# Kernel tuning notes

Hardware: AMD Instinct MI355X
Metric: run time of the kernel (lower is better)

## Reference

```python
import jax, jax.numpy as jnp
import numpy as np

NEG_BIG = 1e20


def setup_inputs() -> dict:
    key = jax.random.key(0)
    k1, k2, k3 = jax.random.split(key, 3)
    B, Tenc, Tdec, D = 8, 2048, 512, 1024
    enc = jax.random.normal(k1, (B, Tenc, D), dtype=jnp.float32)
    dec = jax.random.normal(k2, (B, Tdec, D), dtype=jnp.float32)
    enc_mask = jax.random.randint(k3, (B, Tenc), 0, 2, dtype=jnp.int32)
    # guarantee at least one valid position per row to keep softmax well-defined
    enc_mask = enc_mask.at[:, 0].set(1)
    return {"enc": enc, "enc_mask": enc_mask, "dec": dec}


def reference(enc, enc_mask, dec):
    # dropout=0 and identity transforms -> enc_trans = enc, dec_trans = dec
    mask = enc_mask.astype(enc.dtype)  # (B, Tenc)
    # raw scores: sum_d dec[b,u,d] * enc[b,t,d] -> (B, Tenc, Tdec)
    raw = jnp.einsum('btd,bud->btu', enc, dec)
    raw = raw - (1.0 - mask)[:, :, None] * NEG_BIG
    scores = jax.nn.softmax(raw, axis=1)  # softmax over Tenc
    # context: sum_t scores[b,t,u] * enc[b,t,d] -> (B, Tdec, D)
    context = jnp.einsum('btu,btd->bud', scores, enc)
    return context, scores
```

## Files before the change

### kernel.cpp

```cpp
#include <hip/hip_runtime.h>
#include <math.h>

#define BATCH 8
#define TENC 2048
#define TDEC 512
#define DIM 1024
#define NEG_BIG 1e20f

typedef __attribute__((ext_vector_type(8))) short short8;
typedef __attribute__((ext_vector_type(4))) float f32x4;
typedef unsigned short ushort_t;

__device__ __forceinline__ unsigned int bf16rn(float x) {
    unsigned int u = __float_as_uint(x);
    return (u + 0x7FFFu + ((u >> 16) & 1u)) >> 16;
}
__device__ __forceinline__ float bf16f(unsigned int b) {
    return __uint_as_float(b << 16);
}
__device__ __forceinline__ void split2(float x, unsigned int& h, unsigned int& l) {
    h = bf16rn(x);
    l = bf16rn(x - bf16f(h));
}

#define GLOAD16(g, l)                                                        \
    __builtin_amdgcn_global_load_lds(                                        \
        (const __attribute__((address_space(1))) unsigned int*)(g),          \
        (__attribute__((address_space(3))) unsigned int*)(l), 16, 0, 0)

__device__ __forceinline__ size_t tiled_off(int row, int k, int ntK) {
    return ((size_t)(row >> 4) * ntK + (k >> 5)) * 512
         + ((k >> 3) & 3) * 128 + (row & 15) * 8;
}


__global__ __launch_bounds__(256) void prep_fused(
    const float* __restrict__ enc, const float* __restrict__ dec,
    ushort_t* __restrict__ encH, ushort_t* __restrict__ encL,
    ushort_t* __restrict__ encT, ushort_t* __restrict__ decH,
    ushort_t* __restrict__ decL)
{
    __shared__ ushort_t T[64][72];

    const int b   = blockIdx.z;
    const int d0  = blockIdx.x * 64;
    const int tid = threadIdx.x;

    if (blockIdx.y < 32) {
        const int t0 = blockIdx.y * 64;
        const float* E = enc + (size_t)b * TENC * DIM;
        const size_t bofs1 = (size_t)b * TENC * DIM;
        const size_t bofs2 = (size_t)b * DIM * TENC;

        const int ltr = tid >> 2;
#pragma unroll
        for (int it = 0; it < 2; ++it) {
            const int c  = (tid & 3) + it * 4;
            const int gt = t0 + ltr;
            const int gd = d0 + c * 8;
            float4 x0 = *(const float4*)&E[(size_t)gt * DIM + gd];
            float4 x1 = *(const float4*)&E[(size_t)gt * DIM + gd + 4];
            float xs[8] = {x0.x, x0.y, x0.z, x0.w, x1.x, x1.y, x1.z, x1.w};
            unsigned int h[8], l[8];
            short8 hv, lv;
#pragma unroll
            for (int j = 0; j < 8; ++j) {
                split2(xs[j], h[j], l[j]);
                hv[j] = (short)h[j];
                lv[j] = (short)l[j];
            }
            const size_t off = bofs1 + tiled_off(gt, gd, DIM / 32);
            *(short8*)&encH[off] = hv;
            *(short8*)&encL[off] = lv;
#pragma unroll
            for (int j = 0; j < 8; ++j) T[c * 8 + j][ltr] = (ushort_t)h[j];
        }
        __syncthreads();

        const int dr = tid >> 2;
#pragma unroll
        for (int it = 0; it < 2; ++it) {
            const int tc = (tid & 3) + it * 4;
            const int gd = d0 + dr;
            const int gt = t0 + tc * 8;
            short8 v = *(const short8*)&T[dr][tc * 8];
            *(short8*)&encT[bofs2 + tiled_off(gd, gt, TENC / 32)] = v;
        }
    } else {
        const int u0 = (blockIdx.y - 32) * 64;
        const float* D = dec + (size_t)b * TDEC * DIM;
        const size_t bofs = (size_t)b * TDEC * DIM;

        const int lur = tid >> 2;
#pragma unroll
        for (int it = 0; it < 2; ++it) {
            const int c  = (tid & 3) + it * 4;
            const int gu = u0 + lur;
            const int gd = d0 + c * 8;
            float4 x0 = *(const float4*)&D[(size_t)gu * DIM + gd];
            float4 x1 = *(const float4*)&D[(size_t)gu * DIM + gd + 4];
            float xs[8] = {x0.x, x0.y, x0.z, x0.w, x1.x, x1.y, x1.z, x1.w};
            short8 hv, lv;
#pragma unroll
            for (int j = 0; j < 8; ++j) {
                unsigned int h, l;
                split2(xs[j], h, l);
                hv[j] = (short)h;
                lv[j] = (short)l;
            }
            const size_t off = bofs + tiled_off(gu, gd, DIM / 32);
            *(short8*)&decH[off] = hv;
            *(short8*)&decL[off] = lv;
        }
    }
}

__global__ __launch_bounds__(256) void gemm1_lds(
    const ushort_t* __restrict__ encH, const ushort_t* __restrict__ encL,
    const ushort_t* __restrict__ decH, const ushort_t* __restrict__ decL,
    const int* __restrict__ mask, float* __restrict__ raw,
    float* __restrict__ pm, float* __restrict__ ps)
{
    __shared__ __align__(16) ushort_t Ah[128 * 32];
    __shared__ __align__(16) ushort_t Al[128 * 32];
    __shared__ __align__(16) ushort_t Bh[128 * 32];
    __shared__ __align__(16) ushort_t Bl[128 * 32];
    __shared__ float smx[4][68];
    __shared__ float ssx[4][68];

    const int b  = blockIdx.z;
    const int m0 = blockIdx.y * 128;
    const int n0 = blockIdx.x * 128;
    const int tid = threadIdx.x;

    const int lane = tid & 63;
    const int w    = tid >> 6;
    const int wm   = (w & 1) * 64;
    const int wn   = (w >> 1) * 64;
    const int lr   = lane & 15;
    const int q    = lane >> 4;
    const int l8   = lane * 8;

    const int fa = wm * 32 + q * 128 + lr * 8;
    const int fb = wn * 32 + q * 128 + lr * 8;

    const ushort_t* AH = encH + (size_t)b * TENC * DIM;
    const ushort_t* AL = encL + (size_t)b * TENC * DIM;
    const ushort_t* BH = decH + (size_t)b * TDEC * DIM;
    const ushort_t* BL = decL + (size_t)b * TDEC * DIM;
    float* C = raw + (size_t)b * TENC * TDEC;

    f32x4 acc[4][4] = {};

    for (int k0 = 0; k0 < DIM; k0 += 32) {
        __syncthreads();
#pragma unroll
        for (int q2 = 0; q2 < 2; ++q2) {
            const int rg = w * 2 + q2;
            const size_t tA = ((size_t)((m0 >> 4) + rg) * (DIM / 32) + (k0 >> 5)) * 512 + l8;
            const size_t tB = ((size_t)((n0 >> 4) + rg) * (DIM / 32) + (k0 >> 5)) * 512 + l8;
            GLOAD16(AH + tA, &Ah[rg * 512]);
            GLOAD16(AL + tA, &Al[rg * 512]);
            GLOAD16(BH + tB, &Bh[rg * 512]);
            GLOAD16(BL + tB, &Bl[rg * 512]);
        }
        __syncthreads();

        short8 ah[4], al[4], bh[4], bl[4];
#pragma unroll
        for (int i = 0; i < 4; ++i) {
            ah[i] = *(const short8*)&Ah[fa + i * 512];
            al[i] = *(const short8*)&Al[fa + i * 512];
            bh[i] = *(const short8*)&Bh[fb + i * 512];
            bl[i] = *(const short8*)&Bl[fb + i * 512];
        }
#pragma unroll
        for (int i = 0; i < 4; ++i)
#pragma unroll
            for (int j = 0; j < 4; ++j) {
                acc[i][j] = __builtin_amdgcn_mfma_f32_16x16x32_bf16(ah[i], bh[j], acc[i][j], 0, 0, 0);
                acc[i][j] = __builtin_amdgcn_mfma_f32_16x16x32_bf16(ah[i], bl[j], acc[i][j], 0, 0, 0);
                acc[i][j] = __builtin_amdgcn_mfma_f32_16x16x32_bf16(al[i], bh[j], acc[i][j], 0, 0, 0);
            }
    }

    float mkv[4][4];
#pragma unroll
    for (int i = 0; i < 4; ++i)
#pragma unroll
        for (int rr = 0; rr < 4; ++rr) {
            const int t = m0 + wm + i * 16 + q * 4 + rr;
            mkv[i][rr] = (mask[b * TENC + t] == 0) ? NEG_BIG : 0.0f;
        }

    float cm[4] = {-INFINITY, -INFINITY, -INFINITY, -INFINITY};
    float cs[4] = {0.f, 0.f, 0.f, 0.f};
#pragma unroll
    for (int i = 0; i < 4; ++i)
#pragma unroll
        for (int rr = 0; rr < 4; ++rr) {
            const int t = m0 + wm + i * 16 + q * 4 + rr;
#pragma unroll
            for (int j = 0; j < 4; ++j) {
                const int u = n0 + wn + j * 16 + lr;
                const float v = acc[i][j][rr] - mkv[i][rr];
                C[(size_t)t * TDEC + u] = v;
                cm[j] = fmaxf(cm[j], v);
            }
        }
#pragma unroll
    for (int i = 0; i < 4; ++i)
#pragma unroll
        for (int rr = 0; rr < 4; ++rr)
#pragma unroll
            for (int j = 0; j < 4; ++j)
                cs[j] += __expf(acc[i][j][rr] - mkv[i][rr] - cm[j]);

#pragma unroll
    for (int j = 0; j < 4; ++j) {
#pragma unroll
        for (int d = 16; d < 64; d <<= 1) {
            float om = __shfl_xor(cm[j], d, 64);
            float os = __shfl_xor(cs[j], d, 64);
            float mn = fmaxf(cm[j], om);
            cs[j] = cs[j] * __expf(cm[j] - mn) + os * __expf(om - mn);
            cm[j] = mn;
        }
    }

    if (q == 0) {
#pragma unroll
        for (int j = 0; j < 4; ++j) {
            smx[w][j * 16 + lr] = cm[j];
            ssx[w][j * 16 + lr] = cs[j];
        }
    }
    __syncthreads();
    if (tid < 128) {
        const int col = tid;
        const int wp  = (col >> 6) * 2;
        const int ci  = col & 63;
        const float m1 = smx[wp][ci],     s1 = ssx[wp][ci];
        const float m2 = smx[wp + 1][ci], s2 = ssx[wp + 1][ci];
        const float M = fmaxf(m1, m2);
        const float S = s1 * __expf(m1 - M) + s2 * __expf(m2 - M);
        const int idx = b * TDEC + n0 + col;
        const int tb  = m0 >> 7;
        pm[(size_t)tb * (BATCH * TDEC) + idx] = M;
        ps[(size_t)tb * (BATCH * TDEC) + idx] = S;
    }
}

__global__ __launch_bounds__(256) void norm_kernel(
    float* __restrict__ S, const float* __restrict__ pm,
    const float* __restrict__ ps, ushort_t* __restrict__ scoresT)
{
    __shared__ ushort_t T[64][72];
    __shared__ float cMs[64], cIs[64];

    const int b  = blockIdx.z;
    const int t0 = blockIdx.x * 64;
    const int u0 = blockIdx.y * 64;
    const int tid = threadIdx.x;

    if (tid < 64) {
        const int idx = b * TDEC + u0 + tid;
        float M = -INFINITY;
#pragma unroll
        for (int z = 0; z < 16; ++z)
            M = fmaxf(M, pm[(size_t)z * (BATCH * TDEC) + idx]);
        float s = 0.0f;
#pragma unroll
        for (int z = 0; z < 16; ++z)
            s += ps[(size_t)z * (BATCH * TDEC) + idx] *
                 __expf(pm[(size_t)z * (BATCH * TDEC) + idx] - M);
        cMs[tid] = M;
        cIs[tid] = 1.0f / s;
    }
    __syncthreads();

    const int tr  = tid >> 4;
    const int ucl = (tid & 15) * 4;

    float4 M4 = *(const float4*)&cMs[ucl];
    float4 I4 = *(const float4*)&cIs[ucl];

    float* base = S + (size_t)b * TENC * TDEC;

#pragma unroll
    for (int i = 0; i < 4; ++i) {
        const int t = t0 + tr + 16 * i;
        float4 x = *(const float4*)&base[(size_t)t * TDEC + u0 + ucl];
        float4 p;
        p.x = __expf(x.x - M4.x) * I4.x;
        p.y = __expf(x.y - M4.y) * I4.y;
        p.z = __expf(x.z - M4.z) * I4.z;
        p.w = __expf(x.w - M4.w) * I4.w;
        *(float4*)&base[(size_t)t * TDEC + u0 + ucl] = p;
        const int tloc = tr + 16 * i;
        T[ucl + 0][tloc] = (ushort_t)bf16rn(p.x);
        T[ucl + 1][tloc] = (ushort_t)bf16rn(p.y);
        T[ucl + 2][tloc] = (ushort_t)bf16rn(p.z);
        T[ucl + 3][tloc] = (ushort_t)bf16rn(p.w);
    }
    __syncthreads();

    const size_t bofs = (size_t)b * TDEC * TENC;
    const int ur = tid >> 2;
#pragma unroll
    for (int it = 0; it < 2; ++it) {
        const int tc = (tid & 3) + it * 4;
        const int gu = u0 + ur;
        const int gt = t0 + tc * 8;
        short8 v = *(const short8*)&T[ur][tc * 8];
        *(short8*)&scoresT[bofs + tiled_off(gu, gt, TENC / 32)] = v;
    }
}

__global__ __launch_bounds__(256) void gemm2_lds(
    const ushort_t* __restrict__ scoresT, const ushort_t* __restrict__ encT,
    float* __restrict__ p0, float* __restrict__ p1,
    float* __restrict__ p2, float* __restrict__ p3)
{
    __shared__ __align__(16) ushort_t Ah[128 * 32];
    __shared__ __align__(16) ushort_t Bh[128 * 32];

    const int b  = blockIdx.z >> 2;
    const int ks = blockIdx.z & 3;
    const int m0 = blockIdx.y * 128;
    const int n0 = blockIdx.x * 128;
    const int tid = threadIdx.x;

    const int lane = tid & 63;
    const int w    = tid >> 6;
    const int wm   = (w & 1) * 64;
    const int wn   = (w >> 1) * 64;
    const int lr   = lane & 15;
    const int q    = lane >> 4;
    const int l8   = lane * 8;

    const int fa = wm * 32 + q * 128 + lr * 8;
    const int fb = wn * 32 + q * 128 + lr * 8;

    const ushort_t* A = scoresT + (size_t)b * TDEC * TENC;
    const ushort_t* B = encT    + (size_t)b * DIM * TENC;
    float* Psel = ks == 0 ? p0 : (ks == 1 ? p1 : (ks == 2 ? p2 : p3));
    float* P = Psel + (size_t)b * TDEC * DIM;

    const int kbeg = ks * (TENC / 4);
    const int kend = kbeg + TENC / 4;

    f32x4 acc[4][4] = {};

    for (int k0 = kbeg; k0 < kend; k0 += 32) {
        __syncthreads();
#pragma unroll
        for (int q2 = 0; q2 < 2; ++q2) {
            const int rg = w * 2 + q2;
            const size_t tA = ((size_t)((m0 >> 4) + rg) * (TENC / 32) + (k0 >> 5)) * 512 + l8;
            const size_t tB = ((size_t)((n0 >> 4) + rg) * (TENC / 32) + (k0 >> 5)) * 512 + l8;
            GLOAD16(A + tA, &Ah[rg * 512]);
            GLOAD16(B + tB, &Bh[rg * 512]);
        }
        __syncthreads();

        short8 ah[4], bh[4];
#pragma unroll
        for (int i = 0; i < 4; ++i) {
            ah[i] = *(const short8*)&Ah[fa + i * 512];
            bh[i] = *(const short8*)&Bh[fb + i * 512];
        }
#pragma unroll
        for (int i = 0; i < 4; ++i)
#pragma unroll
            for (int j = 0; j < 4; ++j)
                acc[i][j] = __builtin_amdgcn_mfma_f32_16x16x32_bf16(ah[i], bh[j], acc[i][j], 0, 0, 0);
    }

#pragma unroll
    for (int i = 0; i < 4; ++i)
#pragma unroll
        for (int rr = 0; rr < 4; ++rr) {
            const int u = m0 + wm + i * 16 + q * 4 + rr;
#pragma unroll
            for (int j = 0; j < 4; ++j) {
                const int d = n0 + wn + j * 16 + lr;
                P[(size_t)u * DIM + d] = acc[i][j][rr];
            }
        }
}

__global__ __launch_bounds__(256) void reduce_ctx(
    const float* __restrict__ p0, const float* __restrict__ p1,
    const float* __restrict__ p2, const float* __restrict__ p3,
    float* __restrict__ ctx)
{
    const size_t i4 = ((size_t)blockIdx.x * 256 + threadIdx.x) * 4;
    float4 a = *(const float4*)(p0 + i4);
    float4 b = *(const float4*)(p1 + i4);
    float4 c = *(const float4*)(p2 + i4);
    float4 d = *(const float4*)(p3 + i4);
    float4 o;
    o.x = a.x + b.x + c.x + d.x;
    o.y = a.y + b.y + c.y + d.y;
    o.z = a.z + b.z + c.z + d.z;
    o.w = a.w + b.w + c.w + d.w;
    *(float4*)(ctx + i4) = o;
}


__device__ __forceinline__ void store8(ushort_t* ph, ushort_t* pl,
                                       float4 x0, float4 x1) {
    float xs[8] = {x0.x, x0.y, x0.z, x0.w, x1.x, x1.y, x1.z, x1.w};
    short8 hv, lv;
#pragma unroll
    for (int i = 0; i < 8; ++i) {
        unsigned int h, l;
        split2(xs[i], h, l);
        hv[i] = (short)h;
        lv[i] = (short)l;
    }
    *(short8*)ph = hv;
    *(short8*)pl = lv;
}

__device__ __forceinline__ void wr4(ushort_t* ph, ushort_t* pl, const float* x) {
    unsigned int h[4], l[4];
#pragma unroll
    for (int i = 0; i < 4; ++i) split2(x[i], h[i], l[i]);
    *(uint2*)ph = make_uint2(h[0] | (h[1] << 16), h[2] | (h[3] << 16));
    *(uint2*)pl = make_uint2(l[0] | (l[1] << 16), l[2] | (l[3] << 16));
}

__device__ __forceinline__ short8 frag8B(const ushort_t* p) {
    union { short8 v; uint2 u[2]; } f;
    f.u[0] = *(const uint2*)p;
    f.u[1] = *(const uint2*)(p + 4);
    return f.v;
}

__global__ __launch_bounds__(256) void gemm1_mfma(
    const float* __restrict__ enc, const float* __restrict__ dec,
    const int* __restrict__ mask, float* __restrict__ raw)
{
    __shared__ __align__(16) ushort_t Ah[128 * 32];
    __shared__ __align__(16) ushort_t Al[128 * 32];
    __shared__ __align__(16) ushort_t Bh[128 * 32];
    __shared__ __align__(16) ushort_t Bl[128 * 32];

    const int b  = blockIdx.z;
    const int m0 = blockIdx.y * 128;
    const int n0 = blockIdx.x * 128;
    const int tid = threadIdx.x;

    const float* A  = enc + (size_t)b * TENC * DIM;
    const float* Bg = dec + (size_t)b * TDEC * DIM;
    float*       C  = raw + (size_t)b * TENC * TDEC;

    const int lane = tid & 63;
    const int wv   = tid >> 6;
    const int wm   = (wv & 1) * 64;
    const int wn   = (wv >> 1) * 64;
    const int lr   = lane & 15;
    const int q    = lane >> 4;

    const int r0 = tid >> 2;
    const int c8 = (tid & 3) * 8;

    f32x4 acc[4][4] = {};

    for (int k0 = 0; k0 < DIM; k0 += 32) {
        const float* pa0 = A  + (size_t)(m0 + r0) * DIM + k0 + c8;
        const float* pa1 = A  + (size_t)(m0 + r0 + 64) * DIM + k0 + c8;
        const float* pb0 = Bg + (size_t)(n0 + r0) * DIM + k0 + c8;
        const float* pb1 = Bg + (size_t)(n0 + r0 + 64) * DIM + k0 + c8;
        float4 a0 = *(const float4*)pa0, a0b = *(const float4*)(pa0 + 4);
        float4 a1 = *(const float4*)pa1, a1b = *(const float4*)(pa1 + 4);
        float4 b0 = *(const float4*)pb0, b0b = *(const float4*)(pb0 + 4);
        float4 b1 = *(const float4*)pb1, b1b = *(const float4*)(pb1 + 4);

        __syncthreads();
        store8(&Ah[r0 * 32 + c8],        &Al[r0 * 32 + c8],        a0, a0b);
        store8(&Ah[(r0 + 64) * 32 + c8], &Al[(r0 + 64) * 32 + c8], a1, a1b);
        store8(&Bh[r0 * 32 + c8],        &Bl[r0 * 32 + c8],        b0, b0b);
        store8(&Bh[(r0 + 64) * 32 + c8], &Bl[(r0 + 64) * 32 + c8], b1, b1b);
        __syncthreads();

        short8 ah[4], al[4], bh[4], bl[4];
#pragma unroll
        for (int i = 0; i < 4; ++i) {
            ah[i] = *(const short8*)&Ah[(wm + i * 16 + lr) * 32 + q * 8];
            al[i] = *(const short8*)&Al[(wm + i * 16 + lr) * 32 + q * 8];
            bh[i] = *(const short8*)&Bh[(wn + i * 16 + lr) * 32 + q * 8];
            bl[i] = *(const short8*)&Bl[(wn + i * 16 + lr) * 32 + q * 8];
        }
#pragma unroll
        for (int i = 0; i < 4; ++i)
#pragma unroll
            for (int j = 0; j < 4; ++j) {
                acc[i][j] = __builtin_amdgcn_mfma_f32_16x16x32_bf16(ah[i], bh[j], acc[i][j], 0, 0, 0);
                acc[i][j] = __builtin_amdgcn_mfma_f32_16x16x32_bf16(ah[i], bl[j], acc[i][j], 0, 0, 0);
                acc[i][j] = __builtin_amdgcn_mfma_f32_16x16x32_bf16(al[i], bh[j], acc[i][j], 0, 0, 0);
            }
    }

#pragma unroll
    for (int i = 0; i < 4; ++i)
#pragma unroll
        for (int rr = 0; rr < 4; ++rr) {
            const int t = m0 + wm + i * 16 + q * 4 + rr;
            const float mk = (mask[b * TENC + t] == 0) ? NEG_BIG : 0.0f;
#pragma unroll
            for (int j = 0; j < 4; ++j) {
                const int u = n0 + wn + j * 16 + lr;
                C[(size_t)t * TDEC + u] = acc[i][j][rr] - mk;
            }
        }
}

__global__ __launch_bounds__(256) void softmax_kernel(float* __restrict__ S)
{
    const int b  = blockIdx.y;
    const int u0 = blockIdx.x * 16;
    const int up = threadIdx.x & 15;
    const int tg = threadIdx.x >> 4;

    float* col = S + (size_t)b * TENC * TDEC + u0;

    float m = -INFINITY, s = 0.0f;
    for (int t = tg; t < TENC; t += 16) {
        float x = col[(size_t)t * TDEC + up];
        float mn = fmaxf(m, x);
        s = s * __expf(m - mn) + __expf(x - mn);
        m = mn;
    }

    __shared__ float sm[16][17];
    __shared__ float ss[16][17];
    sm[tg][up] = m;
    ss[tg][up] = s;
    __syncthreads();

    float M = -INFINITY;
#pragma unroll
    for (int j = 0; j < 16; ++j) M = fmaxf(M, sm[j][up]);
    float sum = 0.0f;
#pragma unroll
    for (int j = 0; j < 16; ++j) sum += ss[j][up] * __expf(sm[j][up] - M);
    const float inv = 1.0f / sum;

    for (int t = tg; t < TENC; t += 16) {
        float x = col[(size_t)t * TDEC + up];
        col[(size_t)t * TDEC + up] = __expf(x - M) * inv;
    }
}

#define G2_LD 36

__global__ __launch_bounds__(256) void gemm2_mfma(
    const float* __restrict__ scores, const float* __restrict__ enc,
    float* __restrict__ context)
{
    __shared__ __align__(16) ushort_t Ah[128 * G2_LD];
    __shared__ __align__(16) ushort_t Al[128 * G2_LD];
    __shared__ __align__(16) ushort_t Bh[128 * G2_LD];
    __shared__ __align__(16) ushort_t Bl[128 * G2_LD];

    const int b  = blockIdx.z;
    const int m0 = blockIdx.y * 128;
    const int n0 = blockIdx.x * 128;
    const int tid = threadIdx.x;

    const float* S = scores + (size_t)b * TENC * TDEC;
    const float* E = enc    + (size_t)b * TENC * DIM;
    float*       C = context + (size_t)b * TDEC * DIM;

    const int lane = tid & 63;
    const int wv   = tid >> 6;
    const int wm   = (wv & 1) * 64;
    const int wn   = (wv >> 1) * 64;
    const int lr   = lane & 15;
    const int q    = lane >> 4;

    const int ul = tid & 127;
    const int th = (tid >> 7) * 16;

    f32x4 acc[4][4] = {};

    for (int k0 = 0; k0 < TENC; k0 += 32) {
        float av[16], bv[16];
#pragma unroll
        for (int i = 0; i < 4; ++i) {
            const int t = k0 + th + i * 4;
#pragma unroll
            for (int j = 0; j < 4; ++j) {
                av[i * 4 + j] = S[(size_t)(t + j) * TDEC + m0 + ul];
                bv[i * 4 + j] = E[(size_t)(t + j) * DIM + n0 + ul];
            }
        }
        __syncthreads();
#pragma unroll
        for (int i = 0; i < 4; ++i) {
            const int tt = th + i * 4;
            wr4(&Ah[ul * G2_LD + tt], &Al[ul * G2_LD + tt], &av[i * 4]);
            wr4(&Bh[ul * G2_LD + tt], &Bl[ul * G2_LD + tt], &bv[i * 4]);
        }
        __syncthreads();

        short8 ah[4], al[4], bh[4], bl[4];
#pragma unroll
        for (int i = 0; i < 4; ++i) {
            ah[i] = frag8B(&Ah[(wm + i * 16 + lr) * G2_LD + q * 8]);
            al[i] = frag8B(&Al[(wm + i * 16 + lr) * G2_LD + q * 8]);
            bh[i] = frag8B(&Bh[(wn + i * 16 + lr) * G2_LD + q * 8]);
            bl[i] = frag8B(&Bl[(wn + i * 16 + lr) * G2_LD + q * 8]);
        }
#pragma unroll
        for (int i = 0; i < 4; ++i)
#pragma unroll
            for (int j = 0; j < 4; ++j) {
                acc[i][j] = __builtin_amdgcn_mfma_f32_16x16x32_bf16(ah[i], bh[j], acc[i][j], 0, 0, 0);
                acc[i][j] = __builtin_amdgcn_mfma_f32_16x16x32_bf16(ah[i], bl[j], acc[i][j], 0, 0, 0);
                acc[i][j] = __builtin_amdgcn_mfma_f32_16x16x32_bf16(al[i], bh[j], acc[i][j], 0, 0, 0);
            }
    }

#pragma unroll
    for (int i = 0; i < 4; ++i)
#pragma unroll
        for (int rr = 0; rr < 4; ++rr) {
            const int u = m0 + wm + i * 16 + q * 4 + rr;
#pragma unroll
            for (int j = 0; j < 4; ++j) {
                const int d = n0 + wn + j * 16 + lr;
                C[(size_t)u * DIM + d] = acc[i][j][rr];
            }
        }
}

extern "C" void kernel_launch(void* const* d_in, const int* in_sizes, int n_in,
                              void* d_out, int out_size, void* d_ws, size_t ws_size,
                              hipStream_t stream)
{
    const float* enc      = (const float*)d_in[0];
    const int*   enc_mask = (const int*)  d_in[1];
    const float* dec      = (const float*)d_in[2];

    float* context = (float*)d_out;
    float* scores  = context + (size_t)BATCH * TDEC * DIM;

    const size_t OFF_ENC_H = 0;
    const size_t OFF_ENC_L = 33554432;
    const size_t OFF_DEC_H = 67108864;
    const size_t OFF_DEC_L = 75497472;
    const size_t OFF_ENC_T = 83886080;
    const size_t OFF_SCO_T = 117440512;
    const size_t WS_NEED   = 134217728;

    if (ws_size >= WS_NEED) {
        char* w = (char*)d_ws;
        ushort_t* encH    = (ushort_t*)(w + OFF_ENC_H);
        ushort_t* encL    = (ushort_t*)(w + OFF_ENC_L);
        ushort_t* decH    = (ushort_t*)(w + OFF_DEC_H);
        ushort_t* decL    = (ushort_t*)(w + OFF_DEC_L);
        ushort_t* encT    = (ushort_t*)(w + OFF_ENC_T);
        ushort_t* scoresT = (ushort_t*)(w + OFF_SCO_T);
        float*    part0   = (float*)(w + OFF_ENC_H);
        float*    part1   = (float*)(w + OFF_ENC_H + 16777216);
        float*    part2   = (float*)(w + OFF_ENC_L);
        float*    part3   = (float*)(w + OFF_ENC_L + 16777216);
        float*    pm      = context;
        float*    ps      = context + 65536;

        prep_fused<<<dim3(DIM / 64, 40, BATCH), 256, 0, stream>>>(
            enc, dec, encH, encL, encT, decH, decL);

        gemm1_lds<<<dim3(TDEC / 128, TENC / 128, BATCH), 256, 0, stream>>>(
            encH, encL, decH, decL, enc_mask, scores, pm, ps);

        norm_kernel<<<dim3(TENC / 64, TDEC / 64, BATCH), 256, 0, stream>>>(
            scores, pm, ps, scoresT);

        gemm2_lds<<<dim3(DIM / 128, TDEC / 128, BATCH * 4), 256, 0, stream>>>(
            scoresT, encT, part0, part1, part2, part3);

        reduce_ctx<<<4096, 256, 0, stream>>>(part0, part1, part2, part3, context);
    } else {
        gemm1_mfma<<<dim3(TDEC / 128, TENC / 128, BATCH), 256, 0, stream>>>(
            enc, dec, enc_mask, scores);
        softmax_kernel<<<dim3(TDEC / 16, BATCH), 256, 0, stream>>>(scores);
        gemm2_mfma<<<dim3(DIM / 128, TDEC / 128, BATCH), 256, 0, stream>>>(
            scores, enc, context);
    }
}
```

Measured before the change: 243.3 us.

## Store split-K partials as bf16 and put batch on blockIdx.x

The gemm2 split-K partial sums are now written as bf16, and the reduce kernel reads and sums them as bf16. This halves the traffic for the partial buffers. The launch grids for gemm1 and gemm2 are also reordered so batch is the fastest-varying block index, which is meant to spread batches across XCDs and improve cache locality. The cost is lower precision in the context output, since each partial is rounded to bf16 before the final fp32 sum.

```diff
diff --git a/kernel.cpp b/kernel.cpp
--- a/kernel.cpp
+++ b/kernel.cpp
@@ -128,9 +128,9 @@
     __shared__ float smx[4][68];
     __shared__ float ssx[4][68];
 
-    const int b  = blockIdx.z;
+    const int b  = blockIdx.x;
     const int m0 = blockIdx.y * 128;
-    const int n0 = blockIdx.x * 128;
+    const int n0 = blockIdx.z * 128;
     const int tid = threadIdx.x;
 
     const int lane = tid & 63;
@@ -319,16 +319,16 @@
 
 __global__ __launch_bounds__(256) void gemm2_lds(
     const ushort_t* __restrict__ scoresT, const ushort_t* __restrict__ encT,
-    float* __restrict__ p0, float* __restrict__ p1,
-    float* __restrict__ p2, float* __restrict__ p3)
+    ushort_t* __restrict__ p0, ushort_t* __restrict__ p1,
+    ushort_t* __restrict__ p2, ushort_t* __restrict__ p3)
 {
     __shared__ __align__(16) ushort_t Ah[128 * 32];
     __shared__ __align__(16) ushort_t Bh[128 * 32];
 
-    const int b  = blockIdx.z >> 2;
-    const int ks = blockIdx.z & 3;
-    const int m0 = blockIdx.y * 128;
-    const int n0 = blockIdx.x * 128;
+    const int b  = blockIdx.x;
+    const int ks = blockIdx.y >> 3;
+    const int n0 = (blockIdx.y & 7) * 128;
+    const int m0 = blockIdx.z * 128;
     const int tid = threadIdx.x;
 
     const int lane = tid & 63;
@@ -344,8 +344,8 @@
 
     const ushort_t* A = scoresT + (size_t)b * TDEC * TENC;
     const ushort_t* B = encT    + (size_t)b * DIM * TENC;
-    float* Psel = ks == 0 ? p0 : (ks == 1 ? p1 : (ks == 2 ? p2 : p3));
-    float* P = Psel + (size_t)b * TDEC * DIM;
+    ushort_t* Psel = ks == 0 ? p0 : (ks == 1 ? p1 : (ks == 2 ? p2 : p3));
+    ushort_t* P = Psel + (size_t)b * TDEC * DIM;
 
     const int kbeg = ks * (TENC / 4);
     const int kend = kbeg + TENC / 4;
@@ -385,27 +385,28 @@
 #pragma unroll
             for (int j = 0; j < 4; ++j) {
                 const int d = n0 + wn + j * 16 + lr;
-                P[(size_t)u * DIM + d] = acc[i][j][rr];
+                P[(size_t)u * DIM + d] = (ushort_t)bf16rn(acc[i][j][rr]);
             }
         }
 }
 
 __global__ __launch_bounds__(256) void reduce_ctx(
-    const float* __restrict__ p0, const float* __restrict__ p1,
-    const float* __restrict__ p2, const float* __restrict__ p3,
+    const ushort_t* __restrict__ p0, const ushort_t* __restrict__ p1,
+    const ushort_t* __restrict__ p2, const ushort_t* __restrict__ p3,
     float* __restrict__ ctx)
 {
-    const size_t i4 = ((size_t)blockIdx.x * 256 + threadIdx.x) * 4;
-    float4 a = *(const float4*)(p0 + i4);
-    float4 b = *(const float4*)(p1 + i4);
-    float4 c = *(const float4*)(p2 + i4);
-    float4 d = *(const float4*)(p3 + i4);
-    float4 o;
-    o.x = a.x + b.x + c.x + d.x;
-    o.y = a.y + b.y + c.y + d.y;
-    o.z = a.z + b.z + c.z + d.z;
-    o.w = a.w + b.w + c.w + d.w;
-    *(float4*)(ctx + i4) = o;
+    const size_t i8 = ((size_t)blockIdx.x * 256 + threadIdx.x) * 8;
+    short8 a = *(const short8*)(p0 + i8);
+    short8 b = *(const short8*)(p1 + i8);
+    short8 c = *(const short8*)(p2 + i8);
+    short8 d = *(const short8*)(p3 + i8);
+    float o[8];
+#pragma unroll
+    for (int j = 0; j < 8; ++j)
+        o[j] = bf16f((unsigned short)a[j]) + bf16f((unsigned short)b[j])
+             + bf16f((unsigned short)c[j]) + bf16f((unsigned short)d[j]);
+    *(float4*)(ctx + i8)     = make_float4(o[0], o[1], o[2], o[3]);
+    *(float4*)(ctx + i8 + 4) = make_float4(o[4], o[5], o[6], o[7]);
 }
 
 
@@ -665,26 +666,26 @@
         ushort_t* decL    = (ushort_t*)(w + OFF_DEC_L);
         ushort_t* encT    = (ushort_t*)(w + OFF_ENC_T);
         ushort_t* scoresT = (ushort_t*)(w + OFF_SCO_T);
-        float*    part0   = (float*)(w + OFF_ENC_H);
-        float*    part1   = (float*)(w + OFF_ENC_H + 16777216);
-        float*    part2   = (float*)(w + OFF_ENC_L);
-        float*    part3   = (float*)(w + OFF_ENC_L + 16777216);
+        ushort_t* part0   = (ushort_t*)(w + OFF_ENC_H);
+        ushort_t* part1   = (ushort_t*)(w + OFF_ENC_H + 8388608);
+        ushort_t* part2   = (ushort_t*)(w + OFF_ENC_H + 16777216);
+        ushort_t* part3   = (ushort_t*)(w + OFF_ENC_H + 25165824);
         float*    pm      = context;
         float*    ps      = context + 65536;
 
         prep_fused<<<dim3(DIM / 64, 40, BATCH), 256, 0, stream>>>(
             enc, dec, encH, encL, encT, decH, decL);
 
-        gemm1_lds<<<dim3(TDEC / 128, TENC / 128, BATCH), 256, 0, stream>>>(
+        gemm1_lds<<<dim3(BATCH, TENC / 128, TDEC / 128), 256, 0, stream>>>(
             encH, encL, decH, decL, enc_mask, scores, pm, ps);
 
         norm_kernel<<<dim3(TENC / 64, TDEC / 64, BATCH), 256, 0, stream>>>(
             scores, pm, ps, scoresT);
 
-        gemm2_lds<<<dim3(DIM / 128, TDEC / 128, BATCH * 4), 256, 0, stream>>>(
+        gemm2_lds<<<dim3(BATCH, 32, TDEC / 128), 256, 0, stream>>>(
             scoresT, encT, part0, part1, part2, part3);
 
-        reduce_ctx<<<4096, 256, 0, stream>>>(part0, part1, part2, part3, context);
+        reduce_ctx<<<2048, 256, 0, stream>>>(part0, part1, part2, part3, context);
     } else {
         gemm1_mfma<<<dim3(TDEC / 128, TENC / 128, BATCH), 256, 0, stream>>>(
             enc, dec, enc_mask, scores);
```

Result: faster. 233.2 us (-4.1%).
